# Performance work log

Hardware: AMD Instinct MI355X
Metric: run time of the kernel (lower is better)

The kernel has to match this reference:

```python
import jax, jax.numpy as jnp
import numpy as np

D = 512        # embed_dim
H = 2048       # expert hidden (4*D)
E = 8          # num_experts
TOPK = 2       # num_experts_per_tok


def setup_inputs() -> dict:
    key = jax.random.key(0)
    ks = jax.random.split(key, 5)
    s = 0.02
    x = jax.random.normal(ks[0], (4, 8192, D), dtype=jnp.float32)
    gate_w = jax.random.normal(ks[1], (D, E), dtype=jnp.float32) * s
    W1 = jax.random.normal(ks[2], (E, D, H), dtype=jnp.float32) * s
    W3 = jax.random.normal(ks[3], (E, D, H), dtype=jnp.float32) * s
    W2 = jax.random.normal(ks[4], (E, H, D), dtype=jnp.float32) * s
    return {"x": x, "gate_w": gate_w, "W1": W1, "W2": W2, "W3": W3}


def reference(x, gate_w, W1, W2, W3):
    B, S, _ = x.shape
    xt = x.reshape(-1, D)                      # [T, D]
    T = xt.shape[0]
    gate_logits = xt @ gate_w                  # [T, E]
    w, idx = jax.lax.top_k(gate_logits, TOPK)  # [T, k]
    w = jax.nn.softmax(w, axis=1).astype(xt.dtype)
    # combine weights: comb[t, e] = routing weight of expert e for token t (0 if unselected)
    comb = jnp.zeros((T, E), dtype=xt.dtype).at[jnp.arange(T)[:, None], idx].add(w)
    out = jnp.zeros_like(xt)
    for e in range(E):
        h = jax.nn.silu(xt @ W1[e]) * (xt @ W3[e])   # [T, H]
        out = out + (h @ W2[e]) * comb[:, e:e + 1]
    return out.reshape(B, S, D)
```

## Files before the change

kernel.cpp:

```cpp
#include <hip/hip_runtime.h>
#include <stdint.h>

#define D_DIM 512
#define H_DIM 2048
#define E_NUM 8
#define TOPK_N 2

typedef __attribute__((ext_vector_type(8))) short bf16x8;
typedef __attribute__((ext_vector_type(4))) float f32x4;

#define GLOAD_LDS16(gsrc, ldst)                                                     \
    __builtin_amdgcn_global_load_lds(                                               \
        (const __attribute__((address_space(1))) void*)(gsrc),                      \
        (__attribute__((address_space(3))) void*)(ldst), 16, 0, 0)

static __device__ __forceinline__ unsigned short f2bf(float f) {
    unsigned u = __float_as_uint(f);
    unsigned r = (u + 0x7fffu + ((u >> 16) & 1u)) >> 16;
    return (unsigned short)r;
}

__global__ void init_kernel(int* list_token, float* list_w, unsigned short* zrow, int cap) {
    int id = blockIdx.x * blockDim.x + threadIdx.x;
    if (id < cap) { list_token[id] = -1; list_w[id] = 0.f; }
    if (id < D_DIM) zrow[id] = 0;
}

__global__ void gate_cvt_kernel(const float* __restrict__ x, const float* __restrict__ gw,
                                unsigned short* __restrict__ xb,
                                int* __restrict__ ridx, float* __restrict__ rw, int T) {
    int wave = threadIdx.x >> 6;
    int lane = threadIdx.x & 63;
    int t = blockIdx.x * 4 + wave;
    if (t >= T) return;
    const float* xr = x + (size_t)t * D_DIM + lane * 8;
    float4 a = *(const float4*)xr;
    float4 b = *(const float4*)(xr + 4);
    union { unsigned short s[8]; uint4 v; } o;
    o.s[0] = f2bf(a.x); o.s[1] = f2bf(a.y); o.s[2] = f2bf(a.z); o.s[3] = f2bf(a.w);
    o.s[4] = f2bf(b.x); o.s[5] = f2bf(b.y); o.s[6] = f2bf(b.z); o.s[7] = f2bf(b.w);
    *(uint4*)(xb + (size_t)t * D_DIM + lane * 8) = o.v;
    float xv[8] = {a.x, a.y, a.z, a.w, b.x, b.y, b.z, b.w};
    float acc[8] = {0.f, 0.f, 0.f, 0.f, 0.f, 0.f, 0.f, 0.f};
#pragma unroll
    for (int i = 0; i < 8; ++i) {
        int d = lane * 8 + i;
        float4 g0 = *(const float4*)(gw + d * 8);
        float4 g1 = *(const float4*)(gw + d * 8 + 4);
        acc[0] += xv[i] * g0.x; acc[1] += xv[i] * g0.y; acc[2] += xv[i] * g0.z; acc[3] += xv[i] * g0.w;
        acc[4] += xv[i] * g1.x; acc[5] += xv[i] * g1.y; acc[6] += xv[i] * g1.z; acc[7] += xv[i] * g1.w;
    }
#pragma unroll
    for (int off = 32; off > 0; off >>= 1) {
#pragma unroll
        for (int e = 0; e < 8; ++e) acc[e] += __shfl_xor(acc[e], off, 64);
    }
    if (lane == 0) {
        int e0 = 0; float l0 = acc[0];
#pragma unroll
        for (int e = 1; e < 8; ++e) if (acc[e] > l0) { l0 = acc[e]; e0 = e; }
        int e1 = -1; float l1 = -1e30f;
#pragma unroll
        for (int e = 0; e < 8; ++e) if (e != e0 && acc[e] > l1) { l1 = acc[e]; e1 = e; }
        float w0 = 1.f / (1.f + expf(l1 - l0));
        ridx[t * 2] = e0; ridx[t * 2 + 1] = e1;
        rw[t * 2] = w0;  rw[t * 2 + 1] = 1.f - w0;
    }
}

__global__ void tconv_kernel(const float* __restrict__ in, unsigned short* __restrict__ out,
                             int R, int C) {
    __shared__ float tile[32][33];
    int e = blockIdx.z;
    const float* src = in + (size_t)e * R * C;
    unsigned short* dst = out + (size_t)e * R * C;
    int c = blockIdx.x * 32 + threadIdx.x;
#pragma unroll
    for (int i = 0; i < 4; ++i) {
        int r = blockIdx.y * 32 + threadIdx.y + i * 8;
        tile[threadIdx.y + i * 8][threadIdx.x] = src[(size_t)r * C + c];
    }
    __syncthreads();
    int r2 = blockIdx.y * 32 + threadIdx.x;
#pragma unroll
    for (int i = 0; i < 4; ++i) {
        int c2 = blockIdx.x * 32 + threadIdx.y + i * 8;
        dst[(size_t)c2 * R + r2] = f2bf(tile[threadIdx.x][threadIdx.y + i * 8]);
    }
}

__global__ void hist_kernel(const int* __restrict__ ridx, int* __restrict__ partial, int npairs) {
    __shared__ int cnt[E_NUM];
    if (threadIdx.x < E_NUM) cnt[threadIdx.x] = 0;
    __syncthreads();
    for (int i = blockIdx.x * blockDim.x + threadIdx.x; i < npairs; i += gridDim.x * blockDim.x)
        atomicAdd(&cnt[ridx[i]], 1);
    __syncthreads();
    if (threadIdx.x < E_NUM) partial[blockIdx.x * E_NUM + threadIdx.x] = cnt[threadIdx.x];
}

__global__ void scan_kernel(const int* __restrict__ partial, int* __restrict__ seg,
                            int* __restrict__ block_base) {
    __shared__ int sp[64 * E_NUM];
    __shared__ int segl[E_NUM + 1];
    int tid = threadIdx.x;
    if (tid < 64 * E_NUM) sp[tid] = partial[tid];
    __syncthreads();
    if (tid == 0) {
        int off = 0;
        for (int e = 0; e < E_NUM; ++e) {
            segl[e] = off;
            int c = 0;
            for (int b = 0; b < 64; ++b) c += sp[b * E_NUM + e];
            off += (c + 127) & ~127;
        }
        segl[E_NUM] = off;
    }
    __syncthreads();
    if (tid < E_NUM) {
        int run = segl[tid];
        for (int b = 0; b < 64; ++b) { block_base[b * E_NUM + tid] = run; run += sp[b * E_NUM + tid]; }
        seg[tid] = segl[tid];
        if (tid == 0) seg[E_NUM] = segl[E_NUM];
    }
}

__global__ void scatter_kernel(const int* __restrict__ ridx, const float* __restrict__ rw,
                               const int* __restrict__ block_base,
                               int* __restrict__ list_token, float* __restrict__ list_w, int npairs) {
    __shared__ int base[E_NUM];
    __shared__ int cnt[E_NUM];
    if (threadIdx.x < E_NUM) { base[threadIdx.x] = block_base[blockIdx.x * E_NUM + threadIdx.x]; cnt[threadIdx.x] = 0; }
    __syncthreads();
    for (int i = blockIdx.x * blockDim.x + threadIdx.x; i < npairs; i += gridDim.x * blockDim.x) {
        int e = ridx[i];
        int pos = base[e] + atomicAdd(&cnt[e], 1);
        list_token[pos] = i >> 1;
        list_w[pos] = rw[i];
    }
}

__global__ __launch_bounds__(256) void gemm1_kernel(
    const unsigned short* __restrict__ xb,
    const unsigned short* __restrict__ w1t,
    const unsigned short* __restrict__ w3t,
    const unsigned short* __restrict__ zrow,
    const int* __restrict__ list_token,
    const int* __restrict__ seg,
    unsigned short* __restrict__ hbuf,
    int chunk_base, int MT, int MG) {
    __shared__ short As[128 * 64];
    __shared__ short Bs[128 * 64];

    int bfl = blockIdx.x;
    int xcd = bfl & 7;
    int idx = bfl >> 3;
    int mlocal = idx % MG;
    int yt = idx / MG;
    int mt = mlocal * 8 + xcd;
    if (mt >= MT) return;

    int tid = threadIdx.x;
    int w = tid >> 6, l = tid & 63;
    int m0 = mt * 128;
    int slot0 = chunk_base + m0;
    int n0 = yt * 64;

    int e = 0;
#pragma unroll
    for (int i = 0; i < E_NUM - 1; ++i) if (slot0 >= seg[i + 1]) e = i + 1;
    const unsigned short* b1 = w1t + ((size_t)e * H_DIM + n0) * D_DIM;
    const unsigned short* b3 = w3t + ((size_t)e * H_DIM + n0) * D_DIM;

    int lr8 = l >> 3, p = l & 7;
    const unsigned short* aptr[4];
    const unsigned short* bptr[4];
#pragma unroll
    for (int q = 0; q < 4; ++q) {
        int row = (q * 4 + w) * 8 + lr8;
        int c = p ^ (row & 7);
        int tok = list_token[slot0 + row];
        aptr[q] = (tok >= 0 ? xb + (size_t)tok * D_DIM : zrow) + c * 8;
        bptr[q] = (row < 64 ? b1 + (size_t)row * D_DIM
                            : b3 + (size_t)(row - 64) * D_DIM) + c * 8;
    }

    int wm = (w & 1) * 64;
    int wn = (w >> 1) * 32;
    int lrr = l & 15;
    int lk = (l >> 4) * 8;

    f32x4 acc1[4][2] = {};
    f32x4 acc3[4][2] = {};

    for (int k0 = 0; k0 < D_DIM; k0 += 64) {
#pragma unroll
        for (int q = 0; q < 4; ++q) {
            GLOAD_LDS16(aptr[q] + k0, &As[(q * 4 + w) * 512]);
            GLOAD_LDS16(bptr[q] + k0, &Bs[(q * 4 + w) * 512]);
        }
        __syncthreads();
#pragma unroll
        for (int ks = 0; ks < 64; ks += 32) {
            int cblk = (ks + lk) >> 3;
            bf16x8 af[4], b1f[2], b3f[2];
#pragma unroll
            for (int i = 0; i < 4; ++i) {
                int row = wm + i * 16 + lrr;
                af[i] = *(const bf16x8*)&As[row * 64 + ((cblk ^ (row & 7)) << 3)];
            }
#pragma unroll
            for (int j = 0; j < 2; ++j) {
                int r1 = wn + j * 16 + lrr;
                b1f[j] = *(const bf16x8*)&Bs[r1 * 64 + ((cblk ^ (r1 & 7)) << 3)];
                int r3 = 64 + wn + j * 16 + lrr;
                b3f[j] = *(const bf16x8*)&Bs[r3 * 64 + ((cblk ^ (r3 & 7)) << 3)];
            }
#pragma unroll
            for (int i = 0; i < 4; ++i)
#pragma unroll
                for (int j = 0; j < 2; ++j) {
                    acc1[i][j] = __builtin_amdgcn_mfma_f32_16x16x32_bf16(af[i], b1f[j], acc1[i][j], 0, 0, 0);
                    acc3[i][j] = __builtin_amdgcn_mfma_f32_16x16x32_bf16(af[i], b3f[j], acc3[i][j], 0, 0, 0);
                }
        }
        __syncthreads();
    }

    int lrow0 = (l >> 4) * 4, lcol = l & 15;
#pragma unroll
    for (int i = 0; i < 4; ++i)
#pragma unroll
        for (int j = 0; j < 2; ++j)
#pragma unroll
            for (int r = 0; r < 4; ++r) {
                int row = wm + i * 16 + lrow0 + r;
                int col = wn + j * 16 + lcol;
                float v1 = acc1[i][j][r];
                float v3 = acc3[i][j][r];
                float h = v1 / (1.f + expf(-v1)) * v3;
                hbuf[(size_t)(m0 + row) * H_DIM + n0 + col] = f2bf(h);
            }
}

__global__ __launch_bounds__(256) void gemm2_kernel(
    const unsigned short* __restrict__ hbuf,
    const unsigned short* __restrict__ w2t,
    const int* __restrict__ list_token,
    const float* __restrict__ list_w,
    const int* __restrict__ seg,
    float* __restrict__ out,
    int chunk_base, int MT) {
    __shared__ short As[128 * 64];
    __shared__ short Bs[64 * 64];
    __shared__ int ltok[128];
    __shared__ float lw[128];

    int bfl = blockIdx.x;
    int xcd = bfl & 7;
    int idx = bfl >> 3;
    int yt = idx & 7;
    int mlocal = idx >> 3;
    int mt = mlocal * 8 + xcd;
    if (mt >= MT) return;

    int tid = threadIdx.x;
    int w = tid >> 6, l = tid & 63;
    int m0 = mt * 128;
    int slot0 = chunk_base + m0;
    int n0 = yt * 64;

    if (tid < 128) { ltok[tid] = list_token[slot0 + tid]; lw[tid] = list_w[slot0 + tid]; }

    int e = 0;
#pragma unroll
    for (int i = 0; i < E_NUM - 1; ++i) if (slot0 >= seg[i + 1]) e = i + 1;
    const unsigned short* b2 = w2t + ((size_t)e * D_DIM + n0) * H_DIM;

    int lr8 = l >> 3, p = l & 7;
    const unsigned short* aptr[4];
    const unsigned short* bptr[2];
#pragma unroll
    for (int q = 0; q < 4; ++q) {
        int row = (q * 4 + w) * 8 + lr8;
        int c = p ^ (row & 7);
        aptr[q] = hbuf + (size_t)(m0 + row) * H_DIM + c * 8;
    }
#pragma unroll
    for (int q = 0; q < 2; ++q) {
        int row = (q * 4 + w) * 8 + lr8;
        int c = p ^ (row & 7);
        bptr[q] = b2 + (size_t)row * H_DIM + c * 8;
    }

    int wm = (w & 1) * 64;
    int wn = (w >> 1) * 32;
    int lrr = l & 15;
    int lk = (l >> 4) * 8;

    f32x4 acc[4][2] = {};

    for (int k0 = 0; k0 < H_DIM; k0 += 64) {
#pragma unroll
        for (int q = 0; q < 4; ++q) GLOAD_LDS16(aptr[q] + k0, &As[(q * 4 + w) * 512]);
#pragma unroll
        for (int q = 0; q < 2; ++q) GLOAD_LDS16(bptr[q] + k0, &Bs[(q * 4 + w) * 512]);
        __syncthreads();
#pragma unroll
        for (int ks = 0; ks < 64; ks += 32) {
            int cblk = (ks + lk) >> 3;
            bf16x8 af[4], bf[2];
#pragma unroll
            for (int i = 0; i < 4; ++i) {
                int row = wm + i * 16 + lrr;
                af[i] = *(const bf16x8*)&As[row * 64 + ((cblk ^ (row & 7)) << 3)];
            }
#pragma unroll
            for (int j = 0; j < 2; ++j) {
                int row = wn + j * 16 + lrr;
                bf[j] = *(const bf16x8*)&Bs[row * 64 + ((cblk ^ (row & 7)) << 3)];
            }
#pragma unroll
            for (int i = 0; i < 4; ++i)
#pragma unroll
                for (int j = 0; j < 2; ++j)
                    acc[i][j] = __builtin_amdgcn_mfma_f32_16x16x32_bf16(af[i], bf[j], acc[i][j], 0, 0, 0);
        }
        __syncthreads();
    }

    int lrow0 = (l >> 4) * 4, lcol = l & 15;
#pragma unroll
    for (int i = 0; i < 4; ++i)
#pragma unroll
        for (int j = 0; j < 2; ++j)
#pragma unroll
            for (int r = 0; r < 4; ++r) {
                int row = wm + i * 16 + lrow0 + r;
                int col = wn + j * 16 + lcol;
                int tok = ltok[row];
                if (tok >= 0)
                    atomicAdd(&out[(size_t)tok * D_DIM + n0 + col], acc[i][j][r] * lw[row]);
            }
}

extern "C" void kernel_launch(void* const* d_in, const int* in_sizes, int n_in,
                              void* d_out, int out_size, void* d_ws, size_t ws_size,
                              hipStream_t stream) {
    const float* x  = (const float*)d_in[0];
    const float* gw = (const float*)d_in[1];
    const float* W1 = (const float*)d_in[2];
    const float* W2 = (const float*)d_in[3];
    const float* W3 = (const float*)d_in[4];
    float* out = (float*)d_out;

    int T = in_sizes[0] / D_DIM;
    int npairs = T * TOPK_N;
    const int CAP = npairs + E_NUM * 128;
    const int NCHUNK = 8;
    int chunk_slots = CAP / NCHUNK;
    int MT = chunk_slots / 128;
    int MG = (MT + 7) / 8;

    char* p = (char*)d_ws;
    size_t off = 0;
    auto take = [&](size_t bytes) {
        char* r = p + off;
        off = (off + bytes + 255) & ~(size_t)255;
        return r;
    };
    int* seg           = (int*)take((E_NUM + 1) * 4);
    int* partial       = (int*)take(64 * E_NUM * 4);
    int* block_base    = (int*)take(64 * E_NUM * 4);
    int* list_token    = (int*)take((size_t)CAP * 4);
    float* list_w      = (float*)take((size_t)CAP * 4);
    int* ridx          = (int*)take((size_t)npairs * 4);
    float* rw          = (float*)take((size_t)npairs * 4);
    unsigned short* zrow = (unsigned short*)take((size_t)D_DIM * 2);
    unsigned short* xb  = (unsigned short*)take((size_t)T * D_DIM * 2);
    unsigned short* w1t = (unsigned short*)take((size_t)E_NUM * D_DIM * H_DIM * 2);
    unsigned short* w3t = (unsigned short*)take((size_t)E_NUM * D_DIM * H_DIM * 2);
    unsigned short* w2t = (unsigned short*)take((size_t)E_NUM * D_DIM * H_DIM * 2);
    unsigned short* hbuf = (unsigned short*)take((size_t)chunk_slots * H_DIM * 2);
    (void)ws_size;

    hipMemsetAsync(d_out, 0, (size_t)out_size * sizeof(float), stream);

    init_kernel<<<(CAP + 255) / 256, 256, 0, stream>>>(list_token, list_w, zrow, CAP);

    gate_cvt_kernel<<<T / 4, 256, 0, stream>>>(x, gw, xb, ridx, rw, T);

    dim3 tb(32, 8);
    tconv_kernel<<<dim3(H_DIM / 32, D_DIM / 32, E_NUM), tb, 0, stream>>>(W1, w1t, D_DIM, H_DIM);
    tconv_kernel<<<dim3(H_DIM / 32, D_DIM / 32, E_NUM), tb, 0, stream>>>(W3, w3t, D_DIM, H_DIM);
    tconv_kernel<<<dim3(D_DIM / 32, H_DIM / 32, E_NUM), tb, 0, stream>>>(W2, w2t, H_DIM, D_DIM);

    hist_kernel<<<64, 256, 0, stream>>>(ridx, partial, npairs);
    scan_kernel<<<1, 512, 0, stream>>>(partial, seg, block_base);
    scatter_kernel<<<64, 256, 0, stream>>>(ridx, rw, block_base, list_token, list_w, npairs);

    int g1_grid = 8 * MG * (H_DIM / 64);
    int g2_grid = 8 * (D_DIM / 64) * MG;
    for (int c = 0; c < NCHUNK; ++c) {
        int cb = c * chunk_slots;
        gemm1_kernel<<<g1_grid, 256, 0, stream>>>(
            xb, w1t, w3t, zrow, list_token, seg, hbuf, cb, MT, MG);
        gemm2_kernel<<<g2_grid, 256, 0, stream>>>(
            hbuf, w2t, list_token, list_w, seg, out, cb, MT);
    }
}
```

Baseline: 1.045 ms.

## Widen gemm2 N tile, halve chunk count, transpose gate weights for coalescing

```diff
diff --git a/kernel.cpp b/kernel.cpp
--- a/kernel.cpp
+++ b/kernel.cpp
@@ -26,7 +26,13 @@
     if (id < D_DIM) zrow[id] = 0;
 }
 
-__global__ void gate_cvt_kernel(const float* __restrict__ x, const float* __restrict__ gw,
+__global__ void gwt_kernel(const float* __restrict__ gw, float* __restrict__ gwT) {
+    int id = blockIdx.x * blockDim.x + threadIdx.x;
+    int e = id >> 9, d = id & 511;
+    gwT[id] = gw[d * E_NUM + e];
+}
+
+__global__ void gate_cvt_kernel(const float* __restrict__ x, const float* __restrict__ gwT,
                                 unsigned short* __restrict__ xb,
                                 int* __restrict__ ridx, float* __restrict__ rw, int T) {
     int wave = threadIdx.x >> 6;
@@ -40,15 +46,14 @@
     o.s[0] = f2bf(a.x); o.s[1] = f2bf(a.y); o.s[2] = f2bf(a.z); o.s[3] = f2bf(a.w);
     o.s[4] = f2bf(b.x); o.s[5] = f2bf(b.y); o.s[6] = f2bf(b.z); o.s[7] = f2bf(b.w);
     *(uint4*)(xb + (size_t)t * D_DIM + lane * 8) = o.v;
-    float xv[8] = {a.x, a.y, a.z, a.w, b.x, b.y, b.z, b.w};
-    float acc[8] = {0.f, 0.f, 0.f, 0.f, 0.f, 0.f, 0.f, 0.f};
-#pragma unroll
-    for (int i = 0; i < 8; ++i) {
-        int d = lane * 8 + i;
-        float4 g0 = *(const float4*)(gw + d * 8);
-        float4 g1 = *(const float4*)(gw + d * 8 + 4);
-        acc[0] += xv[i] * g0.x; acc[1] += xv[i] * g0.y; acc[2] += xv[i] * g0.z; acc[3] += xv[i] * g0.w;
-        acc[4] += xv[i] * g1.x; acc[5] += xv[i] * g1.y; acc[6] += xv[i] * g1.z; acc[7] += xv[i] * g1.w;
+    float acc[8];
+#pragma unroll
+    for (int e = 0; e < 8; ++e) {
+        const float* g = gwT + e * D_DIM + lane * 8;
+        float4 g0 = *(const float4*)g;
+        float4 g1 = *(const float4*)(g + 4);
+        acc[e] = a.x * g0.x + a.y * g0.y + a.z * g0.z + a.w * g0.w
+               + b.x * g1.x + b.y * g1.y + b.z * g1.z + b.w * g1.w;
     }
 #pragma unroll
     for (int off = 32; off > 0; off >>= 1) {
@@ -252,15 +257,15 @@
     float* __restrict__ out,
     int chunk_base, int MT) {
     __shared__ short As[128 * 64];
-    __shared__ short Bs[64 * 64];
+    __shared__ short Bs[128 * 64];
     __shared__ int ltok[128];
     __shared__ float lw[128];
 
     int bfl = blockIdx.x;
     int xcd = bfl & 7;
     int idx = bfl >> 3;
-    int yt = idx & 7;
-    int mlocal = idx >> 3;
+    int yt = idx & 3;
+    int mlocal = idx >> 2;
     int mt = mlocal * 8 + xcd;
     if (mt >= MT) return;
 
@@ -268,7 +273,7 @@
     int w = tid >> 6, l = tid & 63;
     int m0 = mt * 128;
     int slot0 = chunk_base + m0;
-    int n0 = yt * 64;
+    int n0 = yt * 128;
 
     if (tid < 128) { ltok[tid] = list_token[slot0 + tid]; lw[tid] = list_w[slot0 + tid]; }
 
@@ -279,51 +284,47 @@
 
     int lr8 = l >> 3, p = l & 7;
     const unsigned short* aptr[4];
-    const unsigned short* bptr[2];
+    const unsigned short* bptr[4];
 #pragma unroll
     for (int q = 0; q < 4; ++q) {
         int row = (q * 4 + w) * 8 + lr8;
         int c = p ^ (row & 7);
         aptr[q] = hbuf + (size_t)(m0 + row) * H_DIM + c * 8;
-    }
-#pragma unroll
-    for (int q = 0; q < 2; ++q) {
-        int row = (q * 4 + w) * 8 + lr8;
-        int c = p ^ (row & 7);
         bptr[q] = b2 + (size_t)row * H_DIM + c * 8;
     }
 
     int wm = (w & 1) * 64;
-    int wn = (w >> 1) * 32;
+    int wn = (w >> 1) * 64;
     int lrr = l & 15;
     int lk = (l >> 4) * 8;
 
-    f32x4 acc[4][2] = {};
+    f32x4 acc[4][4] = {};
 
     for (int k0 = 0; k0 < H_DIM; k0 += 64) {
 #pragma unroll
-        for (int q = 0; q < 4; ++q) GLOAD_LDS16(aptr[q] + k0, &As[(q * 4 + w) * 512]);
-#pragma unroll
-        for (int q = 0; q < 2; ++q) GLOAD_LDS16(bptr[q] + k0, &Bs[(q * 4 + w) * 512]);
+        for (int q = 0; q < 4; ++q) {
+            GLOAD_LDS16(aptr[q] + k0, &As[(q * 4 + w) * 512]);
+            GLOAD_LDS16(bptr[q] + k0, &Bs[(q * 4 + w) * 512]);
+        }
         __syncthreads();
 #pragma unroll
         for (int ks = 0; ks < 64; ks += 32) {
             int cblk = (ks + lk) >> 3;
-            bf16x8 af[4], bf[2];
+            bf16x8 af[4], bf[4];
 #pragma unroll
             for (int i = 0; i < 4; ++i) {
                 int row = wm + i * 16 + lrr;
                 af[i] = *(const bf16x8*)&As[row * 64 + ((cblk ^ (row & 7)) << 3)];
             }
 #pragma unroll
-            for (int j = 0; j < 2; ++j) {
+            for (int j = 0; j < 4; ++j) {
                 int row = wn + j * 16 + lrr;
                 bf[j] = *(const bf16x8*)&Bs[row * 64 + ((cblk ^ (row & 7)) << 3)];
             }
 #pragma unroll
             for (int i = 0; i < 4; ++i)
 #pragma unroll
-                for (int j = 0; j < 2; ++j)
+                for (int j = 0; j < 4; ++j)
                     acc[i][j] = __builtin_amdgcn_mfma_f32_16x16x32_bf16(af[i], bf[j], acc[i][j], 0, 0, 0);
         }
         __syncthreads();
@@ -333,7 +334,7 @@
 #pragma unroll
     for (int i = 0; i < 4; ++i)
 #pragma unroll
-        for (int j = 0; j < 2; ++j)
+        for (int j = 0; j < 4; ++j)
 #pragma unroll
             for (int r = 0; r < 4; ++r) {
                 int row = wm + i * 16 + lrow0 + r;
@@ -357,7 +358,7 @@
     int T = in_sizes[0] / D_DIM;
     int npairs = T * TOPK_N;
     const int CAP = npairs + E_NUM * 128;
-    const int NCHUNK = 8;
+    const int NCHUNK = 4;
     int chunk_slots = CAP / NCHUNK;
     int MT = chunk_slots / 128;
     int MG = (MT + 7) / 8;
@@ -376,6 +377,7 @@
     float* list_w      = (float*)take((size_t)CAP * 4);
     int* ridx          = (int*)take((size_t)npairs * 4);
     float* rw          = (float*)take((size_t)npairs * 4);
+    float* gwT         = (float*)take((size_t)E_NUM * D_DIM * 4);
     unsigned short* zrow = (unsigned short*)take((size_t)D_DIM * 2);
     unsigned short* xb  = (unsigned short*)take((size_t)T * D_DIM * 2);
     unsigned short* w1t = (unsigned short*)take((size_t)E_NUM * D_DIM * H_DIM * 2);
@@ -387,8 +389,9 @@
     hipMemsetAsync(d_out, 0, (size_t)out_size * sizeof(float), stream);
 
     init_kernel<<<(CAP + 255) / 256, 256, 0, stream>>>(list_token, list_w, zrow, CAP);
-
-    gate_cvt_kernel<<<T / 4, 256, 0, stream>>>(x, gw, xb, ridx, rw, T);
+    gwt_kernel<<<(E_NUM * D_DIM) / 256, 256, 0, stream>>>(gw, gwT);
+
+    gate_cvt_kernel<<<T / 4, 256, 0, stream>>>(x, gwT, xb, ridx, rw, T);
 
     dim3 tb(32, 8);
     tconv_kernel<<<dim3(H_DIM / 32, D_DIM / 32, E_NUM), tb, 0, stream>>>(W1, w1t, D_DIM, H_DIM);
@@ -400,7 +403,7 @@
     scatter_kernel<<<64, 256, 0, stream>>>(ridx, rw, block_base, list_token, list_w, npairs);
 
     int g1_grid = 8 * MG * (H_DIM / 64);
-    int g2_grid = 8 * (D_DIM / 64) * MG;
+    int g2_grid = 8 * MG * (D_DIM / 128);
     for (int c = 0; c < NCHUNK; ++c) {
         int cb = c * chunk_slots;
         gemm1_kernel<<<g1_grid, 256, 0, stream>>>(
```

Result: no change. 1.032 ms (-1.3%).
